# Optimization experiments

Hardware: AMD Instinct MI355X
Metric: run time of the kernel (lower is better)

Reference implementation:

```python
import jax, jax.numpy as jnp
import numpy as np

B, L, D = 8, 4096, 256
G, K = 64, 8          # n_groups, group_size
N = G * K             # 512 slots
H = 8                 # attention heads
EPS = 1e-5

def _ln(x, g, b):
    m = jnp.mean(x, axis=-1, keepdims=True)
    v = jnp.var(x, axis=-1, keepdims=True)
    return (x - m) * jax.lax.rsqrt(v + EPS) * g + b

def _gelu(x):
    return jax.nn.gelu(x, approximate=False)  # torch nn.GELU default = exact erf

def setup_inputs() -> dict:
    key = jax.random.key(0)
    ks = jax.random.split(key, 24)
    s = 0.02
    d = {
        'X': jax.random.normal(ks[0], (B, L, D), jnp.float32),
        'S': jax.random.normal(ks[1], (B, N, D), jnp.float32),
        'Wg':  jax.random.normal(ks[2], (D, G)) * s,
        'Wk':  jax.random.normal(ks[3], (D, K)) * s,
        'Wm1': jax.random.normal(ks[4], (D, 2*D)) * s, 'bm1': jnp.zeros((2*D,)),
        'Wm2': jax.random.normal(ks[5], (2*D, D)) * s, 'bm2': jnp.zeros((D,)),
        'Wgt1': jax.random.normal(ks[6], (D, D)) * s, 'bgt1': jnp.zeros((D,)),
        'Wgt2': jax.random.normal(ks[7], (D, 1)) * s, 'bgt2': jnp.zeros((1,)),
        'Wqkv': jax.random.normal(ks[8], (D, 3*D)) * s, 'bqkv': jnp.zeros((3*D,)),
        'Wo':  jax.random.normal(ks[9], (D, D)) * s, 'bo': jnp.zeros((D,)),
        'aln_g': jnp.ones((D,)), 'aln_b': jnp.zeros((D,)),
        'Wu1': jax.random.normal(ks[10], (2*D, 2*D)) * s, 'bu1': jnp.zeros((2*D,)),
        'Wu2': jax.random.normal(ks[11], (2*D, D)) * s, 'bu2': jnp.zeros((D,)),
        'ln_g': jnp.ones((D,)), 'ln_b': jnp.zeros((D,)),
    }
    return d

def reference(X, S, Wg, Wk, Wm1, bm1, Wm2, bm2, Wgt1, bgt1, Wgt2, bgt2,
              Wqkv, bqkv, Wo, bo, aln_g, aln_b, Wu1, bu1, Wu2, bu2, ln_g, ln_b):
    # --- hierarchical routing (eval path: argmax one-hot) ---
    msg = _gelu(X @ Wm1 + bm1) @ Wm2 + bm2                 # (B,L,D)
    gate = jax.nn.sigmoid(_gelu(X @ Wgt1 + bgt1) @ Wgt2 + bgt2)  # (B,L,1)
    gm = msg * gate
    gidx = jnp.argmax(X @ Wg, axis=-1)                     # (B,L)
    kidx = jnp.argmax(X @ Wk, axis=-1)                     # (B,L)
    idx = gidx * K + kidx                                  # flat slot id in [0,N)
    full = jax.nn.one_hot(idx, N, dtype=X.dtype)           # (B,L,N)
    incoming = jnp.einsum('bln,bld->bnd', full, gm)        # (B,N,D)
    # --- slot self-attention ---
    qkv = S @ Wqkv + bqkv
    q, k, v = jnp.split(qkv, 3, axis=-1)
    dh = D // H
    q = q.reshape(B, N, H, dh); k = k.reshape(B, N, H, dh); v = v.reshape(B, N, H, dh)
    scores = jnp.einsum('bqhd,bkhd->bhqk', q, k) / jnp.sqrt(jnp.asarray(dh, X.dtype))
    attn = jax.nn.softmax(scores, axis=-1)
    o = jnp.einsum('bhqk,bkhd->bqhd', attn, v).reshape(B, N, D) @ Wo + bo
    S1 = _ln(S + o, aln_g, aln_b)
    # --- update ---
    cat = jnp.concatenate([S1, incoming], axis=-1)         # (B,N,2D)
    S2 = S1 + _gelu(cat @ Wu1 + bu1) @ Wu2 + bu2
    return _ln(S2, ln_g, ln_b)
```

## Files before the change

kernel.cpp:

```cpp
#include <hip/hip_runtime.h>

typedef __bf16 bf16_t;
typedef __bf16 bf16x8 __attribute__((ext_vector_type(8)));
typedef __bf16 bf16x4v __attribute__((ext_vector_type(4)));
typedef __bf16 bf16x2v __attribute__((ext_vector_type(2)));
typedef float f32x4 __attribute__((ext_vector_type(4)));
typedef unsigned long long u64;

#define LN_EPS 1e-5f

__device__ __forceinline__ float erf_fast(float a) {
  const float t = fabsf(a);
  const float s = a * a;
  float r;
  if (t > 0.921875f) {
    float u;
    r = fmaf(-1.72853470e-5f, t, 3.83197126e-4f);
    u = fmaf(-3.88396438e-3f, t, 2.42546219e-2f);
    r = fmaf(r, s, u);
    r = fmaf(r, t, 1.06777877e-1f);
    r = fmaf(r, t, -6.37245935e-1f);
    r = fmaf(r, t, -1.28717512e-1f);
    r = fmaf(r, t, t);
    r = 1.0f - __expf(-r);
    r = copysignf(r, a);
  } else {
    r = -5.96761703e-4f;
    r = fmaf(r, s, 4.99119423e-3f);
    r = fmaf(r, s, -2.67681349e-2f);
    r = fmaf(r, s, 1.12819925e-1f);
    r = fmaf(r, s, -3.76125336e-1f);
    r = fmaf(r, s, 1.28379166e-1f);
    r = fmaf(r, a, a);
  }
  return r;
}

__device__ __forceinline__ float gelu_f(float x) {
  const float h = 0.5f * x;
  return fmaf(h, erf_fast(x * 0.70710678118654752f), h);
}

__device__ __forceinline__ void async16(const bf16_t* g, bf16_t* l) {
  __builtin_amdgcn_global_load_lds(
      (const __attribute__((address_space(1))) void*)g,
      (__attribute__((address_space(3))) void*)l, 16, 0, 0);
}

__global__ __launch_bounds__(256)
void prep_kernel(const float* __restrict__ X, const float* __restrict__ S,
                 const float* __restrict__ Wg, const float* __restrict__ Wk,
                 const float* __restrict__ Wm1, const float* __restrict__ Wgt1,
                 const float* __restrict__ Wm2, const float* __restrict__ Wqkv,
                 const float* __restrict__ Wo, const float* __restrict__ Wu1,
                 const float* __restrict__ Wu2,
                 bf16_t* __restrict__ Xb, bf16_t* __restrict__ Sb,
                 bf16_t* __restrict__ W1t, bf16_t* __restrict__ W2t,
                 bf16_t* __restrict__ Wqkvt, bf16_t* __restrict__ Wot,
                 bf16_t* __restrict__ Wu1t, bf16_t* __restrict__ Wu2t,
                 float4* __restrict__ zbase)
{
  const int bid = blockIdx.x;
  const int t = threadIdx.x;
  if (bid < 8192) {
    const int i = bid * 256 + t;
    const float4 v = ((const float4*)X)[i];
    bf16x4v o; o[0]=(bf16_t)v.x; o[1]=(bf16_t)v.y; o[2]=(bf16_t)v.z; o[3]=(bf16_t)v.w;
    ((bf16x4v*)Xb)[i] = o;
  } else if (bid < 9216) {
    const int i = (bid - 8192) * 256 + t;
    const float4 v = ((const float4*)S)[i];
    bf16x4v o; o[0]=(bf16_t)v.x; o[1]=(bf16_t)v.y; o[2]=(bf16_t)v.z; o[3]=(bf16_t)v.w;
    ((bf16x4v*)Sb)[i] = o;
  } else if (bid < 10112) {
    const int n = bid - 9216;
    const int k = t;
    float v;
    if (n < 512)      v = Wm1[k * 512 + n];
    else if (n < 768) v = Wgt1[k * 256 + (n - 512)];
    else if (n < 832) v = Wg[k * 64 + (n - 768)];
    else if (n < 840) v = Wk[k * 8 + (n - 832)];
    else              v = 0.f;
    W1t[n * 256 + k] = (bf16_t)v;
  } else if (bid < 10368) {
    const int n = bid - 10112;
    for (int k = t; k < 512; k += 256) W2t[n * 512 + k] = (bf16_t)Wm2[k * 256 + n];
  } else if (bid < 11136) {
    const int n = bid - 10368;
    Wqkvt[n * 256 + t] = (bf16_t)Wqkv[t * 768 + n];
  } else if (bid < 11392) {
    const int n = bid - 11136;
    Wot[n * 256 + t] = (bf16_t)Wo[t * 256 + n];
  } else if (bid < 11904) {
    const int n = bid - 11392;
    for (int k = t; k < 512; k += 256) Wu1t[n * 512 + k] = (bf16_t)Wu1[k * 512 + n];
  } else if (bid < 12160) {
    const int n = bid - 11904;
    for (int k = t; k < 512; k += 256) Wu2t[n * 512 + k] = (bf16_t)Wu2[k * 256 + n];
  } else {
    zbase[(bid - 12160) * 256 + t] = make_float4(0.f, 0.f, 0.f, 0.f);
  }
}

template<int MT, int EPI>
__global__ __launch_bounds__(256)
void gemm_kernel(const bf16_t* __restrict__ A, int lda,
                 const bf16_t* __restrict__ Bt, int K,
                 const float* __restrict__ bias, const float* __restrict__ bias2,
                 void* __restrict__ outp, int ldc,
                 const float* __restrict__ wgt2, float* __restrict__ gatelin,
                 u64* __restrict__ bitmap)
{
  constexpr int BM = MT * 32;
  constexpr int CA = BM * 4;
  const int m0 = blockIdx.x * BM;
  const int by = blockIdx.y;
  const int n0 = by * 128;
  const int t = threadIdx.x;
  const int w = t >> 6;
  const int lane = t & 63;
  const int wr = w >> 1, wc = w & 1;
  const int quad = lane >> 4, l15 = lane & 15;

  __shared__ bf16_t lA[BM * 32];
  __shared__ bf16_t lB[128 * 32];
  __shared__ float sWg[256];
  __shared__ int sKi[BM];

  if constexpr (EPI == 1) {
    if (by >= 4 && by < 6) sWg[t] = wgt2[t];
  }

  f32x4 acc[MT][4];
#pragma unroll
  for (int mt = 0; mt < MT; ++mt)
#pragma unroll
    for (int nt = 0; nt < 4; ++nt)
      acc[mt][nt] = (f32x4){0.f, 0.f, 0.f, 0.f};

  for (int k0 = 0; k0 < K; k0 += 32) {
    if constexpr (CA >= 256) {
#pragma unroll
      for (int i = 0; i < CA / 256; ++i) {
        const int c = i * 256 + t;
        async16(A + (size_t)(m0 + (c >> 2)) * lda + k0 + (c & 3) * 8,
                lA + (size_t)(i * 256 + (t & 192)) * 8);
      }
    } else {
      if (t < CA)
        async16(A + (size_t)(m0 + (t >> 2)) * lda + k0 + (t & 3) * 8,
                lA + (size_t)(t & 192) * 8);
    }
#pragma unroll
    for (int i = 0; i < 2; ++i) {
      const int c = i * 256 + t;
      async16(Bt + (size_t)(n0 + (c >> 2)) * K + k0 + (c & 3) * 8,
              lB + (size_t)(i * 256 + (t & 192)) * 8);
    }
    __syncthreads();
    bf16x8 af[MT], bfr[4];
    const int ko = quad * 8;
#pragma unroll
    for (int mt = 0; mt < MT; ++mt)
      af[mt] = *(const bf16x8*)&lA[(wr * MT * 16 + mt * 16 + l15) * 32 + ko];
#pragma unroll
    for (int nt = 0; nt < 4; ++nt)
      bfr[nt] = *(const bf16x8*)&lB[(wc * 64 + nt * 16 + l15) * 32 + ko];
#pragma unroll
    for (int mt = 0; mt < MT; ++mt)
#pragma unroll
      for (int nt = 0; nt < 4; ++nt)
        acc[mt][nt] = __builtin_amdgcn_mfma_f32_16x16x32_bf16(bfr[nt], af[mt], acc[mt][nt], 0, 0, 0);
    __syncthreads();
  }

  if constexpr (EPI == 1) {
    if (by < 4) {
#pragma unroll
      for (int mt = 0; mt < MT; ++mt) {
        const int row = m0 + wr * MT * 16 + mt * 16 + l15;
#pragma unroll
        for (int nt = 0; nt < 4; ++nt) {
          const int colb = n0 + wc * 64 + nt * 16 + quad * 4;
          const float4 bb = *(const float4*)&bias[colb];
          bf16x4v o;
          o[0] = (bf16_t)gelu_f(acc[mt][nt][0] + bb.x);
          o[1] = (bf16_t)gelu_f(acc[mt][nt][1] + bb.y);
          o[2] = (bf16_t)gelu_f(acc[mt][nt][2] + bb.z);
          o[3] = (bf16_t)gelu_f(acc[mt][nt][3] + bb.w);
          *(bf16x4v*)&((bf16_t*)outp)[(size_t)row * 512 + colb] = o;
        }
      }
    } else if (by < 6) {
#pragma unroll
      for (int mt = 0; mt < MT; ++mt) {
        const int row = m0 + wr * MT * 16 + mt * 16 + l15;
        float part = 0.f;
#pragma unroll
        for (int nt = 0; nt < 4; ++nt) {
          const int colb = n0 + wc * 64 + nt * 16 + quad * 4;
          const int c = colb - 512;
          const float4 bb = *(const float4*)&bias2[c];
          part = fmaf(gelu_f(acc[mt][nt][0] + bb.x), sWg[c + 0], part);
          part = fmaf(gelu_f(acc[mt][nt][1] + bb.y), sWg[c + 1], part);
          part = fmaf(gelu_f(acc[mt][nt][2] + bb.z), sWg[c + 2], part);
          part = fmaf(gelu_f(acc[mt][nt][3] + bb.w), sWg[c + 3], part);
        }
        part += __shfl_xor(part, 16, 64);
        part += __shfl_xor(part, 32, 64);
        if (lane < 16) atomicAdd(&gatelin[row], part);
      }
    } else {
      int bi[MT];
#pragma unroll
      for (int mt = 0; mt < MT; ++mt) {
        if (wc == 0) {
          float mv = -1e30f; int mi = 0;
#pragma unroll
          for (int nt = 0; nt < 4; ++nt)
#pragma unroll
            for (int j = 0; j < 4; ++j) {
              const int gc = nt * 16 + quad * 4 + j;
              const float v = acc[mt][nt][j];
              if (v > mv || (v == mv && gc < mi)) { mv = v; mi = gc; }
            }
#pragma unroll
          for (int off = 16; off <= 32; off <<= 1) {
            const float ov = __shfl_xor(mv, off, 64);
            const int oi = __shfl_xor(mi, off, 64);
            if (ov > mv || (ov == mv && oi < mi)) { mv = ov; mi = oi; }
          }
          bi[mt] = mi;
        } else {
          float mv = -1e30f; int mi = 0;
          if (quad < 2) {
#pragma unroll
            for (int j = 0; j < 4; ++j) {
              const int kc = quad * 4 + j;
              const float v = acc[mt][0][j];
              if (v > mv || (v == mv && kc < mi)) { mv = v; mi = kc; }
            }
          }
#pragma unroll
          for (int off = 16; off <= 32; off <<= 1) {
            const float ov = __shfl_xor(mv, off, 64);
            const int oi = __shfl_xor(mi, off, 64);
            if (ov > mv || (ov == mv && oi < mi)) { mv = ov; mi = oi; }
          }
          if (lane < 16) sKi[wr * MT * 16 + mt * 16 + l15] = mi;
        }
      }
      __syncthreads();
      if (wc == 0 && lane < 16) {
#pragma unroll
        for (int mt = 0; mt < MT; ++mt) {
          const int rl = wr * MT * 16 + mt * 16 + l15;
          const int row = m0 + rl;
          const int idx = bi[mt] * 8 + sKi[rl];
          const int b = row >> 12, tok = row & 4095;
          atomicOr(&bitmap[(size_t)(b * 512 + idx) * 64 + (tok >> 6)],
                   1ull << (tok & 63));
        }
      }
    }
  } else {
#pragma unroll
    for (int mt = 0; mt < MT; ++mt) {
      const int row = m0 + wr * MT * 16 + mt * 16 + l15;
#pragma unroll
      for (int nt = 0; nt < 4; ++nt) {
        const int colb = n0 + wc * 64 + nt * 16 + quad * 4;
        const float4 bb = *(const float4*)&bias[colb];
        bf16x4v o;
        o[0]=(bf16_t)gelu_f(acc[mt][nt][0]+bb.x); o[1]=(bf16_t)gelu_f(acc[mt][nt][1]+bb.y);
        o[2]=(bf16_t)gelu_f(acc[mt][nt][2]+bb.z); o[3]=(bf16_t)gelu_f(acc[mt][nt][3]+bb.w);
        *(bf16x4v*)&((bf16_t*)outp)[(size_t)row * ldc + colb] = o;
      }
    }
  }
}

__global__ __launch_bounds__(256)
void gemm_pair_kernel(const bf16_t* __restrict__ H, const bf16_t* __restrict__ W2t,
                      const float* __restrict__ bm2, const float* __restrict__ sumg,
                      float* __restrict__ incom,
                      const bf16_t* __restrict__ Sb, const bf16_t* __restrict__ Wqkvt,
                      const float* __restrict__ bqkv, bf16_t* __restrict__ qkvb)
{
  int id = blockIdx.x;
  const bool first = id < 256;
  if (!first) id -= 256;
  const bf16_t* A  = first ? H : Sb;
  const bf16_t* Bt = first ? W2t : Wqkvt;
  const float* bias = first ? bm2 : bqkv;
  const int lda = first ? 512 : 256;
  const int K   = first ? 512 : 256;
  const int ldc = first ? 256 : 768;
  const int m0 = (id & 127) * 32;
  const int n0 = (id >> 7) * 128;
  const int t = threadIdx.x;
  const int w = t >> 6;
  const int lane = t & 63;
  const int wr = w >> 1, wc = w & 1;
  const int quad = lane >> 4, l15 = lane & 15;

  __shared__ bf16_t lA[32 * 32];
  __shared__ bf16_t lB[128 * 32];

  f32x4 acc[4];
#pragma unroll
  for (int nt = 0; nt < 4; ++nt) acc[nt] = (f32x4){0.f, 0.f, 0.f, 0.f};

  for (int k0 = 0; k0 < K; k0 += 32) {
    if (t < 128)
      async16(A + (size_t)(m0 + (t >> 2)) * lda + k0 + (t & 3) * 8,
              lA + (size_t)(t & 192) * 8);
#pragma unroll
    for (int i = 0; i < 2; ++i) {
      const int c = i * 256 + t;
      async16(Bt + (size_t)(n0 + (c >> 2)) * K + k0 + (c & 3) * 8,
              lB + (size_t)(i * 256 + (t & 192)) * 8);
    }
    __syncthreads();
    bf16x8 af, bfr[4];
    const int ko = quad * 8;
    af = *(const bf16x8*)&lA[(wr * 16 + l15) * 32 + ko];
#pragma unroll
    for (int nt = 0; nt < 4; ++nt)
      bfr[nt] = *(const bf16x8*)&lB[(wc * 64 + nt * 16 + l15) * 32 + ko];
#pragma unroll
    for (int nt = 0; nt < 4; ++nt)
      acc[nt] = __builtin_amdgcn_mfma_f32_16x16x32_bf16(bfr[nt], af, acc[nt], 0, 0, 0);
    __syncthreads();
  }

  const int row = m0 + wr * 16 + l15;
  if (first) {
    const float gt = sumg[row];
#pragma unroll
    for (int nt = 0; nt < 4; ++nt) {
      const int colb = n0 + wc * 64 + nt * 16 + quad * 4;
      const float4 bb = *(const float4*)&bias[colb];
      *(float4*)&incom[(size_t)row * ldc + colb] =
          make_float4(fmaf(gt, bb.x, acc[nt][0]), fmaf(gt, bb.y, acc[nt][1]),
                      fmaf(gt, bb.z, acc[nt][2]), fmaf(gt, bb.w, acc[nt][3]));
    }
  } else {
#pragma unroll
    for (int nt = 0; nt < 4; ++nt) {
      const int colb = n0 + wc * 64 + nt * 16 + quad * 4;
      const float4 bb = *(const float4*)&bias[colb];
      bf16x4v o; o[0]=(bf16_t)(acc[nt][0]+bb.x); o[1]=(bf16_t)(acc[nt][1]+bb.y);
      o[2]=(bf16_t)(acc[nt][2]+bb.z); o[3]=(bf16_t)(acc[nt][3]+bb.w);
      *(bf16x4v*)&qkvb[(size_t)row * ldc + colb] = o;
    }
  }
}

__global__ __launch_bounds__(256)
void gather_kernel(const bf16_t* __restrict__ h1, const float* __restrict__ gatelin,
                   const float* __restrict__ bgt2, const u64* __restrict__ bitmap,
                   bf16_t* __restrict__ H, float* __restrict__ sumg)
{
  const int bs = blockIdx.x;
  const int b = bs >> 9;
  const int t = threadIdx.x;
  __shared__ u64 sw[64];
  if (t < 64) sw[t] = bitmap[(size_t)bs * 64 + t];
  __syncthreads();
  const float bg = bgt2[0];
  float a0 = 0.f, a1 = 0.f, sg = 0.f;
  for (int wd = 0; wd < 64; ++wd) {
    u64 word = sw[wd];
    while (word) {
      const int bit = __builtin_ctzll(word);
      word &= word - 1;
      const int l = (b << 12) + (wd << 6) + bit;
      const float g = 1.0f / (1.0f + __expf(-(gatelin[l] + bg)));
      const bf16x2v hv = *(const bf16x2v*)&h1[(size_t)l * 512 + t * 2];
      a0 = fmaf(g, (float)hv[0], a0);
      a1 = fmaf(g, (float)hv[1], a1);
      sg += g;
    }
  }
  bf16x2v o; o[0] = (bf16_t)a0; o[1] = (bf16_t)a1;
  *(bf16x2v*)&H[(size_t)bs * 512 + t * 2] = o;
  if (t == 0) sumg[bs] = sg;
}

__global__ __launch_bounds__(256)
void attn_kernel(const bf16_t* __restrict__ qkv, bf16_t* __restrict__ obuf)
{
  const int bid = blockIdx.x;
  const int qc = bid & 15;
  const int h = (bid >> 4) & 7;
  const int b = bid >> 7;
  const int t = threadIdx.x;
  const int w = t >> 6, lane = t & 63;
  const int quad = lane >> 4, l15 = lane & 15;

  __shared__ bf16_t sP[32 * 520];
  __shared__ bf16_t sVt[32 * 264];
  __shared__ float sL[32];

  bf16x8 qf[2];
#pragma unroll
  for (int mt = 0; mt < 2; ++mt) {
    const int row = b * 512 + qc * 32 + mt * 16 + l15;
    qf[mt] = *(const bf16x8*)&qkv[(size_t)row * 768 + h * 32 + quad * 8];
  }
  const float scale = 0.17677669529663687f;
  for (int kt = w; kt < 32; kt += 4) {
    const int key = b * 512 + kt * 16 + l15;
    const bf16x8 kf = *(const bf16x8*)&qkv[(size_t)key * 768 + 256 + h * 32 + quad * 8];
#pragma unroll
    for (int mt = 0; mt < 2; ++mt) {
      f32x4 c = (f32x4){0.f, 0.f, 0.f, 0.f};
      c = __builtin_amdgcn_mfma_f32_16x16x32_bf16(qf[mt], kf, c, 0, 0, 0);
#pragma unroll
      for (int r = 0; r < 4; ++r)
        sP[(mt * 16 + quad * 4 + r) * 520 + kt * 16 + l15] = (bf16_t)(c[r] * scale);
    }
  }
  __syncthreads();

#pragma unroll
  for (int ri = 0; ri < 8; ++ri) {
    const int row = w * 8 + ri;
    const bf16x8 sv = *(const bf16x8*)&sP[row * 520 + lane * 8];
    float sval[8];
    float mx = -1e30f;
#pragma unroll
    for (int j = 0; j < 8; ++j) { sval[j] = (float)sv[j]; mx = fmaxf(mx, sval[j]); }
#pragma unroll
    for (int off = 32; off; off >>= 1) mx = fmaxf(mx, __shfl_xor(mx, off, 64));
    float sum = 0.f;
    bf16x8 pv;
#pragma unroll
    for (int j = 0; j < 8; ++j) { const float e = __expf(sval[j] - mx); sum += e; pv[j] = (bf16_t)e; }
#pragma unroll
    for (int off = 32; off; off >>= 1) sum += __shfl_xor(sum, off, 64);
    *(bf16x8*)&sP[row * 520 + lane * 8] = pv;
    if (lane == 0) sL[row] = sum;
  }
  __syncthreads();

  const int omt = w >> 1, ont = w & 1;
  f32x4 oacc = (f32x4){0.f, 0.f, 0.f, 0.f};
  for (int half = 0; half < 2; ++half) {
    if (half) __syncthreads();
#pragma unroll
    for (int i = 0; i < 32; ++i) {
      const int el = i * 256 + t;
      const int dh = el & 31, key = el >> 5;
      sVt[dh * 264 + key] = qkv[(size_t)(b * 512 + half * 256 + key) * 768 + 512 + h * 32 + dh];
    }
    __syncthreads();
#pragma unroll
    for (int kt = 0; kt < 8; ++kt) {
      const bf16x8 af = *(const bf16x8*)&sP[(omt * 16 + l15) * 520 + half * 256 + kt * 32 + quad * 8];
      const bf16x8 vf = *(const bf16x8*)&sVt[(ont * 16 + l15) * 264 + kt * 32 + quad * 8];
      oacc = __builtin_amdgcn_mfma_f32_16x16x32_bf16(af, vf, oacc, 0, 0, 0);
    }
  }
#pragma unroll
  for (int r = 0; r < 4; ++r) {
    const int row = omt * 16 + quad * 4 + r;
    const float val = oacc[r] / sL[row];
    obuf[(size_t)(b * 512 + qc * 32 + row) * 256 + h * 32 + ont * 16 + l15] = (bf16_t)val;
  }
}

__global__ __launch_bounds__(256)
void wo_ln1_kernel(const bf16_t* __restrict__ obuf, const bf16_t* __restrict__ Wot,
                   const float* __restrict__ bo, const float* __restrict__ S,
                   const float* __restrict__ incom, const float* __restrict__ g,
                   const float* __restrict__ bb, float* __restrict__ S1f,
                   bf16_t* __restrict__ A4)
{
  const int m0 = blockIdx.x * 16;
  const int t = threadIdx.x;
  const int w = t >> 6, lane = t & 63;
  const int quad = lane >> 4, l15 = lane & 15;

  __shared__ bf16_t lA[16 * 32];
  __shared__ bf16_t lB[256 * 32];
  __shared__ float sSum[4][16];
  __shared__ float sSq[4][16];

  f32x4 acc[4];
#pragma unroll
  for (int nt = 0; nt < 4; ++nt) acc[nt] = (f32x4){0.f, 0.f, 0.f, 0.f};

  for (int k0 = 0; k0 < 256; k0 += 32) {
    if (t < 64)
      async16(obuf + (size_t)(m0 + (t >> 2)) * 256 + k0 + (t & 3) * 8, lA);
#pragma unroll
    for (int i = 0; i < 4; ++i) {
      const int c = i * 256 + t;
      async16(Wot + (size_t)(c >> 2) * 256 + k0 + (c & 3) * 8,
              lB + (size_t)(i * 256 + (t & 192)) * 8);
    }
    __syncthreads();
    const int ko = quad * 8;
    const bf16x8 af = *(const bf16x8*)&lA[l15 * 32 + ko];
#pragma unroll
    for (int nt = 0; nt < 4; ++nt) {
      const bf16x8 bfr = *(const bf16x8*)&lB[(w * 64 + nt * 16 + l15) * 32 + ko];
      acc[nt] = __builtin_amdgcn_mfma_f32_16x16x32_bf16(bfr, af, acc[nt], 0, 0, 0);
    }
    __syncthreads();
  }

  const int row = m0 + l15;
  float sum = 0.f, sq = 0.f;
#pragma unroll
  for (int nt = 0; nt < 4; ++nt) {
    const int colb = w * 64 + nt * 16 + quad * 4;
    const float4 bv = *(const float4*)&bo[colb];
    const float4 sv = *(const float4*)&S[(size_t)row * 256 + colb];
    float x0 = acc[nt][0] + bv.x + sv.x, x1 = acc[nt][1] + bv.y + sv.y;
    float x2 = acc[nt][2] + bv.z + sv.z, x3 = acc[nt][3] + bv.w + sv.w;
    acc[nt][0] = x0; acc[nt][1] = x1; acc[nt][2] = x2; acc[nt][3] = x3;
    sum += x0 + x1 + x2 + x3;
    sq += x0*x0 + x1*x1 + x2*x2 + x3*x3;
  }
  sum += __shfl_xor(sum, 16, 64); sum += __shfl_xor(sum, 32, 64);
  sq  += __shfl_xor(sq, 16, 64);  sq  += __shfl_xor(sq, 32, 64);
  if (lane < 16) { sSum[w][l15] = sum; sSq[w][l15] = sq; }
  __syncthreads();
  const float tot = sSum[0][l15] + sSum[1][l15] + sSum[2][l15] + sSum[3][l15];
  const float tq  = sSq[0][l15] + sSq[1][l15] + sSq[2][l15] + sSq[3][l15];
  const float mean = tot * 0.00390625f;
  const float var = tq * 0.00390625f - mean * mean;
  const float rstd = rsqrtf(var + LN_EPS);
#pragma unroll
  for (int nt = 0; nt < 4; ++nt) {
    const int colb = w * 64 + nt * 16 + quad * 4;
    const float4 gg = *(const float4*)&g[colb];
    const float4 bv = *(const float4*)&bb[colb];
    const float y0 = (acc[nt][0]-mean)*rstd*gg.x + bv.x;
    const float y1 = (acc[nt][1]-mean)*rstd*gg.y + bv.y;
    const float y2 = (acc[nt][2]-mean)*rstd*gg.z + bv.z;
    const float y3 = (acc[nt][3]-mean)*rstd*gg.w + bv.w;
    *(float4*)&S1f[(size_t)row * 256 + colb] = make_float4(y0, y1, y2, y3);
    bf16x4v yb; yb[0]=(bf16_t)y0; yb[1]=(bf16_t)y1; yb[2]=(bf16_t)y2; yb[3]=(bf16_t)y3;
    *(bf16x4v*)&A4[(size_t)row * 512 + colb] = yb;
    const float4 ic = *(const float4*)&incom[(size_t)row * 256 + colb];
    bf16x4v ib; ib[0]=(bf16_t)ic.x; ib[1]=(bf16_t)ic.y; ib[2]=(bf16_t)ic.z; ib[3]=(bf16_t)ic.w;
    *(bf16x4v*)&A4[(size_t)row * 512 + 256 + colb] = ib;
  }
}

__global__ __launch_bounds__(256)
void wu2_ln2_kernel(const bf16_t* __restrict__ U, const bf16_t* __restrict__ Wu2t,
                    const float* __restrict__ bu2, const float* __restrict__ S1f,
                    const float* __restrict__ g, const float* __restrict__ bb,
                    float* __restrict__ out)
{
  const int m0 = blockIdx.x * 16;
  const int t = threadIdx.x;
  const int w = t >> 6, lane = t & 63;
  const int quad = lane >> 4, l15 = lane & 15;

  __shared__ bf16_t lA[16 * 32];
  __shared__ bf16_t lB[256 * 32];
  __shared__ float sSum[4][16];
  __shared__ float sSq[4][16];

  f32x4 acc[4];
#pragma unroll
  for (int nt = 0; nt < 4; ++nt) acc[nt] = (f32x4){0.f, 0.f, 0.f, 0.f};

  for (int k0 = 0; k0 < 512; k0 += 32) {
    if (t < 64)
      async16(U + (size_t)(m0 + (t >> 2)) * 512 + k0 + (t & 3) * 8, lA);
#pragma unroll
    for (int i = 0; i < 4; ++i) {
      const int c = i * 256 + t;
      async16(Wu2t + (size_t)(c >> 2) * 512 + k0 + (c & 3) * 8,
              lB + (size_t)(i * 256 + (t & 192)) * 8);
    }
    __syncthreads();
    const int ko = quad * 8;
    const bf16x8 af = *(const bf16x8*)&lA[l15 * 32 + ko];
#pragma unroll
    for (int nt = 0; nt < 4; ++nt) {
      const bf16x8 bfr = *(const bf16x8*)&lB[(w * 64 + nt * 16 + l15) * 32 + ko];
      acc[nt] = __builtin_amdgcn_mfma_f32_16x16x32_bf16(bfr, af, acc[nt], 0, 0, 0);
    }
    __syncthreads();
  }

  const int row = m0 + l15;
  float sum = 0.f, sq = 0.f;
#pragma unroll
  for (int nt = 0; nt < 4; ++nt) {
    const int colb = w * 64 + nt * 16 + quad * 4;
    const float4 bv = *(const float4*)&bu2[colb];
    const float4 sv = *(const float4*)&S1f[(size_t)row * 256 + colb];
    float x0 = acc[nt][0] + bv.x + sv.x, x1 = acc[nt][1] + bv.y + sv.y;
    float x2 = acc[nt][2] + bv.z + sv.z, x3 = acc[nt][3] + bv.w + sv.w;
    acc[nt][0] = x0; acc[nt][1] = x1; acc[nt][2] = x2; acc[nt][3] = x3;
    sum += x0 + x1 + x2 + x3;
    sq += x0*x0 + x1*x1 + x2*x2 + x3*x3;
  }
  sum += __shfl_xor(sum, 16, 64); sum += __shfl_xor(sum, 32, 64);
  sq  += __shfl_xor(sq, 16, 64);  sq  += __shfl_xor(sq, 32, 64);
  if (lane < 16) { sSum[w][l15] = sum; sSq[w][l15] = sq; }
  __syncthreads();
  const float tot = sSum[0][l15] + sSum[1][l15] + sSum[2][l15] + sSum[3][l15];
  const float tq  = sSq[0][l15] + sSq[1][l15] + sSq[2][l15] + sSq[3][l15];
  const float mean = tot * 0.00390625f;
  const float var = tq * 0.00390625f - mean * mean;
  const float rstd = rsqrtf(var + LN_EPS);
#pragma unroll
  for (int nt = 0; nt < 4; ++nt) {
    const int colb = w * 64 + nt * 16 + quad * 4;
    const float4 gg = *(const float4*)&g[colb];
    const float4 bv = *(const float4*)&bb[colb];
    *(float4*)&out[(size_t)row * 256 + colb] = make_float4(
        (acc[nt][0]-mean)*rstd*gg.x + bv.x, (acc[nt][1]-mean)*rstd*gg.y + bv.y,
        (acc[nt][2]-mean)*rstd*gg.z + bv.z, (acc[nt][3]-mean)*rstd*gg.w + bv.w);
  }
}

extern "C" void kernel_launch(void* const* d_in, const int* in_sizes, int n_in,
                              void* d_out, int out_size, void* d_ws, size_t ws_size,
                              hipStream_t stream)
{
  (void)in_sizes; (void)n_in; (void)out_size; (void)ws_size;
  const float* X    = (const float*)d_in[0];
  const float* S    = (const float*)d_in[1];
  const float* Wg   = (const float*)d_in[2];
  const float* Wk   = (const float*)d_in[3];
  const float* Wm1  = (const float*)d_in[4];
  const float* bm1  = (const float*)d_in[5];
  const float* Wm2  = (const float*)d_in[6];
  const float* bm2  = (const float*)d_in[7];
  const float* Wgt1 = (const float*)d_in[8];
  const float* bgt1 = (const float*)d_in[9];
  const float* Wgt2 = (const float*)d_in[10];
  const float* bgt2 = (const float*)d_in[11];
  const float* Wqkv = (const float*)d_in[12];
  const float* bqkv = (const float*)d_in[13];
  const float* Wo   = (const float*)d_in[14];
  const float* bo   = (const float*)d_in[15];
  const float* alng = (const float*)d_in[16];
  const float* alnb = (const float*)d_in[17];
  const float* Wu1  = (const float*)d_in[18];
  const float* bu1  = (const float*)d_in[19];
  const float* Wu2  = (const float*)d_in[20];
  const float* bu2  = (const float*)d_in[21];
  const float* lng  = (const float*)d_in[22];
  const float* lnb  = (const float*)d_in[23];

  char* p = (char*)d_ws;
  auto carve = [&](size_t bytes) { char* r = p; p += bytes; return r; };
  bf16_t* Xb    = (bf16_t*)carve(16777216);
  bf16_t* Sb    = (bf16_t*)carve(2097152);
  bf16_t* W1t   = (bf16_t*)carve(458752);
  bf16_t* W2t   = (bf16_t*)carve(262144);
  bf16_t* Wqkvt = (bf16_t*)carve(393216);
  bf16_t* Wot   = (bf16_t*)carve(131072);
  bf16_t* Wu1t  = (bf16_t*)carve(524288);
  bf16_t* Wu2t  = (bf16_t*)carve(262144);
  bf16_t* h1    = (bf16_t*)carve(33554432);
  u64*    bitmap  = (u64*)carve(2097152);
  float*  gatelin = (float*)carve(131072);
  float*  incom = (float*)carve(4194304);
  bf16_t* qkvb  = (bf16_t*)carve(6291456);
  bf16_t* obuf  = (bf16_t*)carve(2097152);
  float*  S1f   = (float*)carve(4194304);
  bf16_t* A4    = (bf16_t*)carve(4194304);
  bf16_t* U     = (bf16_t*)carve(4194304);
  float*  sumg  = (float*)carve(16384);
  bf16_t* H = U;

  prep_kernel<<<12704, 256, 0, stream>>>(X, S, Wg, Wk, Wm1, Wgt1, Wm2, Wqkv, Wo, Wu1, Wu2,
                                         Xb, Sb, W1t, W2t, Wqkvt, Wot, Wu1t, Wu2t,
                                         (float4*)bitmap);
  gemm_kernel<2,1><<<dim3(512,7), 256, 0, stream>>>(Xb, 256, W1t, 256, bm1, bgt1, h1, 512,
                                                    Wgt2, gatelin, bitmap);
  gather_kernel<<<4096, 256, 0, stream>>>(h1, gatelin, bgt2, bitmap, H, sumg);
  gemm_pair_kernel<<<1024, 256, 0, stream>>>(H, W2t, bm2, sumg, incom,
                                             Sb, Wqkvt, bqkv, qkvb);
  attn_kernel<<<1024, 256, 0, stream>>>(qkvb, obuf);
  wo_ln1_kernel<<<256, 256, 0, stream>>>(obuf, Wot, bo, S, incom, alng, alnb, S1f, A4);
  gemm_kernel<1,5><<<dim3(128,4), 256, 0, stream>>>(A4, 512, Wu1t, 512, bu1, nullptr, U, 512,
                                                    nullptr, nullptr, nullptr);
  wu2_ln2_kernel<<<256, 256, 0, stream>>>(U, Wu2t, bu2, S1f, lng, lnb, (float*)d_out);
}
```

Baseline: 260.9 us.

## Swizzle LDS tiles in GEMMs and move GELU into scatter aggregation

Applies an XOR swizzle to the 16-byte chunk position within each 32-element LDS row, in both the async global-to-LDS loads and the fragment reads of every GEMM kernel, to reduce LDS bank conflicts. The GELU on the first MLP layer is removed from the GEMM epilogue and applied instead when the scatter kernel reads h1 for each routed token. This shortens the GEMM epilogue but applies GELU to bf16-rounded pre-activations, which slightly changes numerics.

```diff
diff --git a/kernel.cpp b/kernel.cpp
--- a/kernel.cpp
+++ b/kernel.cpp
@@ -46,6 +46,8 @@
       (const __attribute__((address_space(1))) void*)g,
       (__attribute__((address_space(3))) void*)l, 16, 0, 0);
 }
+
+__device__ __forceinline__ int swz(int row, int p) { return p ^ ((row >> 1) & 3); }
 
 __global__ __launch_bounds__(256)
 void prep_kernel(const float* __restrict__ X, const float* __restrict__ S,
@@ -143,29 +145,36 @@
 #pragma unroll
       for (int i = 0; i < CA / 256; ++i) {
         const int c = i * 256 + t;
-        async16(A + (size_t)(m0 + (c >> 2)) * lda + k0 + (c & 3) * 8,
+        const int row = c >> 2, pp = c & 3;
+        async16(A + (size_t)(m0 + row) * lda + k0 + (swz(row, pp) << 3),
                 lA + (size_t)(i * 256 + (t & 192)) * 8);
       }
     } else {
-      if (t < CA)
-        async16(A + (size_t)(m0 + (t >> 2)) * lda + k0 + (t & 3) * 8,
+      if (t < CA) {
+        const int row = t >> 2, pp = t & 3;
+        async16(A + (size_t)(m0 + row) * lda + k0 + (swz(row, pp) << 3),
                 lA + (size_t)(t & 192) * 8);
+      }
     }
 #pragma unroll
     for (int i = 0; i < 2; ++i) {
       const int c = i * 256 + t;
-      async16(Bt + (size_t)(n0 + (c >> 2)) * K + k0 + (c & 3) * 8,
+      const int row = c >> 2, pp = c & 3;
+      async16(Bt + (size_t)(n0 + row) * K + k0 + (swz(row, pp) << 3),
               lB + (size_t)(i * 256 + (t & 192)) * 8);
     }
     __syncthreads();
     bf16x8 af[MT], bfr[4];
-    const int ko = quad * 8;
-#pragma unroll
-    for (int mt = 0; mt < MT; ++mt)
-      af[mt] = *(const bf16x8*)&lA[(wr * MT * 16 + mt * 16 + l15) * 32 + ko];
-#pragma unroll
-    for (int nt = 0; nt < 4; ++nt)
-      bfr[nt] = *(const bf16x8*)&lB[(wc * 64 + nt * 16 + l15) * 32 + ko];
+#pragma unroll
+    for (int mt = 0; mt < MT; ++mt) {
+      const int row = wr * MT * 16 + mt * 16 + l15;
+      af[mt] = *(const bf16x8*)&lA[row * 32 + (swz(row, quad) << 3)];
+    }
+#pragma unroll
+    for (int nt = 0; nt < 4; ++nt) {
+      const int row = wc * 64 + nt * 16 + l15;
+      bfr[nt] = *(const bf16x8*)&lB[row * 32 + (swz(row, quad) << 3)];
+    }
 #pragma unroll
     for (int mt = 0; mt < MT; ++mt)
 #pragma unroll
@@ -184,10 +193,10 @@
           const int colb = n0 + wc * 64 + nt * 16 + quad * 4;
           const float4 bb = *(const float4*)&bias[colb];
           bf16x4v o;
-          o[0] = (bf16_t)gelu_f(acc[mt][nt][0] + bb.x);
-          o[1] = (bf16_t)gelu_f(acc[mt][nt][1] + bb.y);
-          o[2] = (bf16_t)gelu_f(acc[mt][nt][2] + bb.z);
-          o[3] = (bf16_t)gelu_f(acc[mt][nt][3] + bb.w);
+          o[0] = (bf16_t)(acc[mt][nt][0] + bb.x);
+          o[1] = (bf16_t)(acc[mt][nt][1] + bb.y);
+          o[2] = (bf16_t)(acc[mt][nt][2] + bb.z);
+          o[3] = (bf16_t)(acc[mt][nt][3] + bb.w);
           *(bf16x4v*)&((bf16_t*)outp)[(size_t)row * 512 + colb] = o;
         }
       }
@@ -312,22 +321,27 @@
   for (int nt = 0; nt < 4; ++nt) acc[nt] = (f32x4){0.f, 0.f, 0.f, 0.f};
 
   for (int k0 = 0; k0 < K; k0 += 32) {
-    if (t < 128)
-      async16(A + (size_t)(m0 + (t >> 2)) * lda + k0 + (t & 3) * 8,
+    if (t < 128) {
+      const int row = t >> 2, pp = t & 3;
+      async16(A + (size_t)(m0 + row) * lda + k0 + (swz(row, pp) << 3),
               lA + (size_t)(t & 192) * 8);
+    }
 #pragma unroll
     for (int i = 0; i < 2; ++i) {
       const int c = i * 256 + t;
-      async16(Bt + (size_t)(n0 + (c >> 2)) * K + k0 + (c & 3) * 8,
+      const int row = c >> 2, pp = c & 3;
+      async16(Bt + (size_t)(n0 + row) * K + k0 + (swz(row, pp) << 3),
               lB + (size_t)(i * 256 + (t & 192)) * 8);
     }
     __syncthreads();
     bf16x8 af, bfr[4];
-    const int ko = quad * 8;
-    af = *(const bf16x8*)&lA[(wr * 16 + l15) * 32 + ko];
-#pragma unroll
-    for (int nt = 0; nt < 4; ++nt)
-      bfr[nt] = *(const bf16x8*)&lB[(wc * 64 + nt * 16 + l15) * 32 + ko];
+    const int arow = wr * 16 + l15;
+    af = *(const bf16x8*)&lA[arow * 32 + (swz(arow, quad) << 3)];
+#pragma unroll
+    for (int nt = 0; nt < 4; ++nt) {
+      const int row = wc * 64 + nt * 16 + l15;
+      bfr[nt] = *(const bf16x8*)&lB[row * 32 + (swz(row, quad) << 3)];
+    }
 #pragma unroll
     for (int nt = 0; nt < 4; ++nt)
       acc[nt] = __builtin_amdgcn_mfma_f32_16x16x32_bf16(bfr[nt], af, acc[nt], 0, 0, 0);
@@ -378,8 +392,8 @@
       const int l = (b << 12) + (wd << 6) + bit;
       const float g = 1.0f / (1.0f + __expf(-(gatelin[l] + bg)));
       const bf16x2v hv = *(const bf16x2v*)&h1[(size_t)l * 512 + t * 2];
-      a0 = fmaf(g, (float)hv[0], a0);
-      a1 = fmaf(g, (float)hv[1], a1);
+      a0 = fmaf(g, gelu_f((float)hv[0]), a0);
+      a1 = fmaf(g, gelu_f((float)hv[1]), a1);
       sg += g;
     }
   }
@@ -493,20 +507,23 @@
   for (int nt = 0; nt < 4; ++nt) acc[nt] = (f32x4){0.f, 0.f, 0.f, 0.f};
 
   for (int k0 = 0; k0 < 256; k0 += 32) {
-    if (t < 64)
-      async16(obuf + (size_t)(m0 + (t >> 2)) * 256 + k0 + (t & 3) * 8, lA);
+    if (t < 64) {
+      const int row = t >> 2, pp = t & 3;
+      async16(obuf + (size_t)(m0 + row) * 256 + k0 + (swz(row, pp) << 3), lA);
+    }
 #pragma unroll
     for (int i = 0; i < 4; ++i) {
       const int c = i * 256 + t;
-      async16(Wot + (size_t)(c >> 2) * 256 + k0 + (c & 3) * 8,
+      const int row = c >> 2, pp = c & 3;
+      async16(Wot + (size_t)row * 256 + k0 + (swz(row, pp) << 3),
               lB + (size_t)(i * 256 + (t & 192)) * 8);
     }
     __syncthreads();
-    const int ko = quad * 8;
-    const bf16x8 af = *(const bf16x8*)&lA[l15 * 32 + ko];
+    const bf16x8 af = *(const bf16x8*)&lA[l15 * 32 + (swz(l15, quad) << 3)];
 #pragma unroll
     for (int nt = 0; nt < 4; ++nt) {
-      const bf16x8 bfr = *(const bf16x8*)&lB[(w * 64 + nt * 16 + l15) * 32 + ko];
+      const int row = w * 64 + nt * 16 + l15;
+      const bf16x8 bfr = *(const bf16x8*)&lB[row * 32 + (swz(row, quad) << 3)];
       acc[nt] = __builtin_amdgcn_mfma_f32_16x16x32_bf16(bfr, af, acc[nt], 0, 0, 0);
     }
     __syncthreads();
@@ -573,20 +590,23 @@
   for (int nt = 0; nt < 4; ++nt) acc[nt] = (f32x4){0.f, 0.f, 0.f, 0.f};
 
   for (int k0 = 0; k0 < 512; k0 += 32) {
-    if (t < 64)
-      async16(U + (size_t)(m0 + (t >> 2)) * 512 + k0 + (t & 3) * 8, lA);
+    if (t < 64) {
+      const int row = t >> 2, pp = t & 3;
+      async16(U + (size_t)(m0 + row) * 512 + k0 + (swz(row, pp) << 3), lA);
+    }
 #pragma unroll
     for (int i = 0; i < 4; ++i) {
       const int c = i * 256 + t;
-      async16(Wu2t + (size_t)(c >> 2) * 512 + k0 + (c & 3) * 8,
+      const int row = c >> 2, pp = c & 3;
+      async16(Wu2t + (size_t)row * 512 + k0 + (swz(row, pp) << 3),
               lB + (size_t)(i * 256 + (t & 192)) * 8);
     }
     __syncthreads();
-    const int ko = quad * 8;
-    const bf16x8 af = *(const bf16x8*)&lA[l15 * 32 + ko];
+    const bf16x8 af = *(const bf16x8*)&lA[l15 * 32 + (swz(l15, quad) << 3)];
 #pragma unroll
     for (int nt = 0; nt < 4; ++nt) {
-      const bf16x8 bfr = *(const bf16x8*)&lB[(w * 64 + nt * 16 + l15) * 32 + ko];
+      const int row = w * 64 + nt * 16 + l15;
+      const bf16x8 bfr = *(const bf16x8*)&lB[row * 32 + (swz(row, quad) << 3)];
       acc[nt] = __builtin_amdgcn_mfma_f32_16x16x32_bf16(bfr, af, acc[nt], 0, 0, 0);
     }
     __syncthreads();
```

New measurement: 264.7 us. No clear change (+1.4%).
